# Kernel tuning notes

Measured on AMD Instinct MI355X. Metric: run time of the kernel, lower is better.

The kernel has to match this reference:

```python
import jax, jax.numpy as jnp
import numpy as np

B, C, H, W = 4, 256, 64, 64
GROUPS = 32
EPS = 1e-6
N_BITS_QKV = 8
N_BITS_SM = 8


def setup_inputs() -> dict:
    key = jax.random.key(0)
    ks = jax.random.split(key, 6)
    s = 1.0 / np.sqrt(C)
    return {
        "x": jax.random.normal(ks[0], (B, C, H, W), jnp.float32),
        "gn_scale": jnp.ones((C,), jnp.float32),
        "gn_bias": jnp.zeros((C,), jnp.float32),
        "wq": jax.random.normal(ks[1], (C, C), jnp.float32) * s,
        "bq": jnp.zeros((C,), jnp.float32),
        "wk": jax.random.normal(ks[2], (C, C), jnp.float32) * s,
        "bk": jnp.zeros((C,), jnp.float32),
        "wv": jax.random.normal(ks[3], (C, C), jnp.float32) * s,
        "bv": jnp.zeros((C,), jnp.float32),
        "wproj": jax.random.normal(ks[4], (C, C), jnp.float32) * s,
        "bproj": jnp.zeros((C,), jnp.float32),
        # per-tensor uniform-affine quantizer params (delta, zero_point)
        "dq": jnp.float32(8.0 / 255.0), "zq": jnp.float32(128.0),
        "dk": jnp.float32(8.0 / 255.0), "zk": jnp.float32(128.0),
        "dv": jnp.float32(8.0 / 255.0), "zv": jnp.float32(128.0),
        "dw": jnp.float32(1.0 / 255.0), "zw": jnp.float32(0.0),
    }


def ste_round(x):
    # round with straight-through gradient (as in round_ste of BRECQ/QDrop)
    return x + jax.lax.stop_gradient(jnp.round(x) - x)


def fake_quant(x, delta, zero_point, n_bits):
    # UniformAffineQuantizer: quant -> clamp -> dequant
    n_levels = 2 ** n_bits
    x_int = ste_round(x / delta) + zero_point
    x_q = jnp.clip(x_int, 0, n_levels - 1)
    return (x_q - zero_point) * delta


def group_norm(x, scale, bias):
    b, c, h, w = x.shape
    xg = x.reshape(b, GROUPS, (c // GROUPS) * h * w)
    mu = xg.mean(-1, keepdims=True)
    var = xg.var(-1, keepdims=True)
    xn = ((xg - mu) * jax.lax.rsqrt(var + EPS)).reshape(b, c, h, w)
    return xn * scale[None, :, None, None] + bias[None, :, None, None]


def conv1x1(x, w, b):
    # 1x1 conv == channel-mixing matmul
    return jnp.einsum('bchw,oc->bohw', x, w) + b[None, :, None, None]


def reference(x, gn_scale, gn_bias, wq, bq, wk, bk, wv, bv, wproj, bproj,
              dq, zq, dk, zk, dv, zv, dw, zw):
    h_ = group_norm(x, gn_scale, gn_bias)
    q = conv1x1(h_, wq, bq)
    k = conv1x1(h_, wk, bk)
    v = conv1x1(h_, wv, bv)
    b, c, h, w = q.shape
    hw = h * w
    q = q.reshape(b, c, hw).transpose(0, 2, 1)   # [b, hw, c]
    k = k.reshape(b, c, hw)                      # [b, c, hw]
    q = fake_quant(q, dq, zq, N_BITS_QKV)
    k = fake_quant(k, dk, zk, N_BITS_QKV)
    attn = jnp.einsum('bnc,bcm->bnm', q, k) * (c ** -0.5)  # [b, hw, hw]
    attn = jax.nn.softmax(attn, axis=2)
    v = fake_quant(v.reshape(b, c, hw), dv, zv, N_BITS_QKV)
    attn = fake_quant(attn.transpose(0, 2, 1), dw, zw, N_BITS_SM)  # [b, m, n]
    h_out = jnp.einsum('bcm,bmn->bcn', v, attn).reshape(b, c, h, w)
    return x + conv1x1(h_out, wproj, bproj)
```

## Files before the change

kernel.cpp:

```cpp
#include <hip/hip_runtime.h>


#define Bb 4
#define Cc 256
#define Nn 4096
#define NGRP 32
#define LOG2E 1.4426950408889634f

typedef unsigned short u16;
typedef unsigned int   u32;
typedef unsigned char  u8;
typedef __attribute__((ext_vector_type(8))) short bf16x8;
typedef __attribute__((ext_vector_type(4))) float f32x4;
typedef __attribute__((ext_vector_type(4))) int   i32x4;

#define MFMA16(a,b,c)    __builtin_amdgcn_mfma_f32_16x16x32_bf16((a),(b),(c),0,0,0)
#define MFMA_I8(a,b,c)   __builtin_amdgcn_mfma_i32_16x16x64_i8((a),(b),(c),0,0,0)

static __device__ __forceinline__ u16 f2bf(float x){
  u32 u = __float_as_uint(x);
  u += 0x7fffu + ((u >> 16) & 1u);
  return (u16)(u >> 16);
}
static __device__ __forceinline__ float bf2f(u16 h){ return __uint_as_float(((u32)h) << 16); }

union U64c { u16 u[4]; uint2 v; };

__global__ __launch_bounds__(256) void k_gn_stats(const float* __restrict__ x,
                                                  float* __restrict__ mu, float* __restrict__ rs){
  int bg = blockIdx.x;
  const float4* p = (const float4*)(x + (size_t)bg * (8 * Nn));
  float s = 0.f, q = 0.f;
  for (int i = threadIdx.x; i < 8*Nn/4; i += 256){
    float4 v = p[i];
    s += v.x + v.y + v.z + v.w;
    q += v.x*v.x + v.y*v.y + v.z*v.z + v.w*v.w;
  }
  __shared__ float rsum[256], rsq[256];
  rsum[threadIdx.x] = s; rsq[threadIdx.x] = q;
  __syncthreads();
  for (int off = 128; off > 0; off >>= 1){
    if (threadIdx.x < off){ rsum[threadIdx.x] += rsum[threadIdx.x+off]; rsq[threadIdx.x] += rsq[threadIdx.x+off]; }
    __syncthreads();
  }
  if (threadIdx.x == 0){
    const float inv = 1.0f / (8*Nn);
    float m = rsum[0]*inv;
    float var = rsq[0]*inv - m*m;
    mu[bg] = m; rs[bg] = rsqrtf(var + 1e-6f);
  }
}

__global__ __launch_bounds__(256) void k_wsplit(const float* __restrict__ wq, const float* __restrict__ wk,
                                                const float* __restrict__ wv, const float* __restrict__ wp,
                                                u16* __restrict__ WH, u16* __restrict__ WL){
  int gid = blockIdx.x*256 + threadIdx.x;
  int mat = gid >> 16, idx = gid & 65535;
  const float* src = (mat == 0) ? wq : (mat == 1) ? wk : (mat == 2) ? wv : wp;
  float w = src[idx];
  u16 h = f2bf(w);
  WH[gid] = h;
  WL[gid] = f2bf(w - bf2f(h));
}

__global__ __launch_bounds__(256) void k_gn_apply(const float* __restrict__ x,
                                                  const float* __restrict__ gsc, const float* __restrict__ gbi,
                                                  const float* __restrict__ mu, const float* __restrict__ rs,
                                                  u16* __restrict__ hhi, u16* __restrict__ hlo){
  int nt = blockIdx.x, ct = blockIdx.y, b = blockIdx.z;
  int n0 = nt*64, c0 = ct*64;
  __shared__ float yt[64*65];
  __shared__ float sa[64], sb[64];
  int t = threadIdx.x;
  if (t < 64){
    int c = c0 + t;
    int bg = b*NGRP + (c >> 3);
    float a = rs[bg] * gsc[c];
    sa[t] = a;
    sb[t] = gbi[c] - mu[bg]*a;
  }
  __syncthreads();
  #pragma unroll
  for (int j = 0; j < 4; ++j){
    int id = t + j*256;
    int r = id >> 4, cq = id & 15;
    float4 v = *(const float4*)(x + ((size_t)b*Cc + c0 + r)*Nn + n0 + cq*4);
    float a = sa[r], bb = sb[r];
    yt[r*65 + cq*4 + 0] = v.x*a + bb;
    yt[r*65 + cq*4 + 1] = v.y*a + bb;
    yt[r*65 + cq*4 + 2] = v.z*a + bb;
    yt[r*65 + cq*4 + 3] = v.w*a + bb;
  }
  __syncthreads();
  int nl = t >> 2, cg = (t & 3) * 16;
  size_t base = ((size_t)b*Nn + n0 + nl)*Cc + c0 + cg;
  #pragma unroll
  for (int half = 0; half < 2; ++half){
    union { u16 u[8]; uint4 v; } Ph, Pl;
    #pragma unroll
    for (int u = 0; u < 8; ++u){
      float y = yt[(cg + half*8 + u)*65 + nl];
      u16 h = f2bf(y);
      Ph.u[u] = h; Pl.u[u] = f2bf(y - bf2f(h));
    }
    *(uint4*)(hhi + base + half*8) = Ph.v;
    *(uint4*)(hlo + base + half*8) = Pl.v;
  }
}

__global__ __launch_bounds__(256) void k_convqkv(const u16* __restrict__ WH, const u16* __restrict__ WL,
                                                 const u16* __restrict__ Hhi, const u16* __restrict__ Hlo,
                                                 const float* __restrict__ bq, const float* __restrict__ bk,
                                                 const float* __restrict__ bv,
                                                 const float* __restrict__ dq, const float* __restrict__ zq,
                                                 const float* __restrict__ dk, const float* __restrict__ zk,
                                                 const float* __restrict__ dv, const float* __restrict__ zv,
                                                 u8* __restrict__ qT8, u8* __restrict__ kT8,
                                                 u8* __restrict__ v8){
  int nt = blockIdx.x, ot = blockIdx.y, b = blockIdx.z;
  __shared__ u16 Lh[64*256], Ll[64*256];
  int t = threadIdx.x, lane = t & 63, wave = t >> 6;
  int lo16 = lane & 15, quad = lane >> 4;
  int o0 = ot*64 + wave*16;

  {
    const u16* hb = Hhi + ((size_t)b*Nn + nt*64) * 256;
    const u16* lb = Hlo + ((size_t)b*Nn + nt*64) * 256;
    #pragma unroll
    for (int j = 0; j < 8; ++j){
      int id = t + j*256;
      int r = id >> 5, ch = id & 31;
      int sw = (ch ^ (r & 15)) * 8;
      *(uint4*)(Lh + r*256 + sw) = *(const uint4*)(hb + (size_t)r*256 + ch*8);
      *(uint4*)(Ll + r*256 + sw) = *(const uint4*)(lb + (size_t)r*256 + ch*8);
    }
  }
  __syncthreads();

  const float* Bs[3] = {bq, bk, bv};
  const float* Dsr[3] = {dq, dk, dv};
  const float* Zs[3] = {zq, zk, zv};

  #pragma unroll
  for (int ws = 0; ws < 3; ++ws){
    bf16x8 awh[8], awl[8];
    {
      const u16* wbh = WH + (size_t)ws*65536 + (size_t)(o0 + lo16) * 256 + quad*8;
      const u16* wbl = WL + (size_t)ws*65536 + (size_t)(o0 + lo16) * 256 + quad*8;
      #pragma unroll
      for (int k = 0; k < 8; ++k){
        awh[k] = *(const bf16x8*)(wbh + k*32);
        awl[k] = *(const bf16x8*)(wbl + k*32);
      }
    }
    f32x4 zf = {0.f,0.f,0.f,0.f};
    f32x4 acc[4] = {zf, zf, zf, zf};
    #pragma unroll
    for (int k = 0; k < 8; ++k){
      #pragma unroll
      for (int ns = 0; ns < 4; ++ns){
        int r = ns*16 + lo16;
        int ph = ((k*4 + quad) ^ (r & 15)) * 8;
        bf16x8 bh = *(const bf16x8*)(Lh + r*256 + ph);
        bf16x8 bl = *(const bf16x8*)(Ll + r*256 + ph);
        acc[ns] = MFMA16(awh[k], bh, acc[ns]);
        acc[ns] = MFMA16(awl[k], bh, acc[ns]);
        acc[ns] = MFMA16(awh[k], bl, acc[ns]);
      }
    }
    float bia[4];
    #pragma unroll
    for (int r = 0; r < 4; ++r) bia[r] = Bs[ws][o0 + quad*4 + r];
    float z = Zs[ws][0]; float invd = 1.0f / Dsr[ws][0];

    if (ws < 2){
      u8* outT = (ws == 0) ? qT8 : kT8;
      #pragma unroll
      for (int ns = 0; ns < 4; ++ns){
        int n = nt*64 + ns*16 + lo16;
        u32 w = 0;
        #pragma unroll
        for (int r = 0; r < 4; ++r){
          float v = acc[ns][r] + bia[r];
          float xq = fminf(fmaxf(rintf(v*invd) + z, 0.f), 255.f);
          int qi = (int)rintf(xq - z);
          w |= ((u32)(qi & 255)) << (8*r);
        }
        *(u32*)(outT + ((size_t)b*Nn + n)*Cc + o0 + quad*4) = w;
      }
    } else {
      #pragma unroll
      for (int ns = 0; ns < 4; ++ns){
        int n = nt*64 + ns*16 + lo16;
        #pragma unroll
        for (int r = 0; r < 4; ++r){
          float v = acc[ns][r] + bia[r];
          float xq = fminf(fmaxf(rintf(v*invd) + z, 0.f), 255.f);
          int qi = (int)rintf(xq - z);
          v8[((size_t)b*Cc + o0 + quad*4 + r)*Nn + n] = (u8)(qi & 255);
        }
      }
    }
  }
}

__global__ __launch_bounds__(256) void k_conv(const u16* __restrict__ WH, const u16* __restrict__ WL,
                                              const u16* __restrict__ Hh,
                                              const float* __restrict__ bias,
                                              const float* __restrict__ xres, float* __restrict__ outF){
  int nt = blockIdx.x, ot = blockIdx.y, b = blockIdx.z;
  __shared__ u16 Lh[64*128];
  int t = threadIdx.x, lane = t & 63, wave = t >> 6;
  int lo16 = lane & 15, quad = lane >> 4;
  int o0 = ot*64 + wave*16;

  bf16x8 awh[8], awl[8];
  {
    const u16* wbh = WH + (size_t)3*65536 + (size_t)(o0 + lo16) * 256 + quad*8;
    const u16* wbl = WL + (size_t)3*65536 + (size_t)(o0 + lo16) * 256 + quad*8;
    #pragma unroll
    for (int k = 0; k < 8; ++k){
      awh[k] = *(const bf16x8*)(wbh + k*32);
      awl[k] = *(const bf16x8*)(wbl + k*32);
    }
  }
  f32x4 zf = {0.f,0.f,0.f,0.f};
  f32x4 acc[4] = {zf, zf, zf, zf};

  const u16* hb = Hh + ((size_t)b*Nn + nt*64) * 256;
  for (int kc = 0; kc < 2; ++kc){
    __syncthreads();
    for (int id = t; id < 64*16; id += 256){
      int r = id >> 4, ch = id & 15;
      int sw = (ch ^ (r & 7)) * 8;
      *(uint4*)(Lh + r*128 + sw) = *(const uint4*)(hb + (size_t)r*256 + kc*128 + ch*8);
    }
    __syncthreads();
    #pragma unroll
    for (int k4 = 0; k4 < 4; ++k4){
      int k = kc*4 + k4;
      #pragma unroll
      for (int ns = 0; ns < 4; ++ns){
        int r = ns*16 + lo16;
        int ch = ((k4*4 + quad) ^ (r & 7)) * 8;
        bf16x8 bh = *(const bf16x8*)(Lh + r*128 + ch);
        acc[ns] = MFMA16(awh[k], bh, acc[ns]);
        acc[ns] = MFMA16(awl[k], bh, acc[ns]);
      }
    }
  }

  float bia[4];
  #pragma unroll
  for (int r = 0; r < 4; ++r) bia[r] = bias[o0 + quad*4 + r];
  #pragma unroll
  for (int ns = 0; ns < 4; ++ns){
    int n = nt*64 + ns*16 + lo16;
    #pragma unroll
    for (int r = 0; r < 4; ++r){
      size_t a = ((size_t)b*Cc + o0 + quad*4 + r)*Nn + n;
      outF[a] = xres[a] + acc[ns][r] + bia[r];
    }
  }
}

static __device__ __forceinline__ int sq4(u32 w){
  int s = 0;
  #pragma unroll
  for (int j = 0; j < 4; ++j){ int v = (int)((signed char)((w >> (8*j)) & 0xffu)); s += v*v; }
  return s;
}
static __device__ __forceinline__ int ssum4(u32 w){
  return ((int)(w << 24) >> 24) + ((int)(w << 16) >> 24) + ((int)(w << 8) >> 24) + ((int)w >> 24);
}
__global__ __launch_bounds__(256) void k_normvs(const u8* __restrict__ qT8, const u8* __restrict__ kT8,
                                                const u8* __restrict__ v8,
                                                u32* __restrict__ stat, int* __restrict__ vsum){
  if (blockIdx.x < 128){
    int gid = blockIdx.x*256 + threadIdx.x;
    int which = gid >> 14;
    int rid = gid & 16383;
    const u8* row = (which ? kT8 : qT8) + (size_t)rid * 256;
    u32 acc = 0;
    const uint4* p = (const uint4*)row;
    #pragma unroll
    for (int i = 0; i < 16; ++i){
      uint4 w = p[i];
      acc += (u32)(sq4(w.x) + sq4(w.y) + sq4(w.z) + sq4(w.w));
    }
    #pragma unroll
    for (int msk = 32; msk > 0; msk >>= 1){
      u32 o = (u32)__shfl_xor((int)acc, msk, 64);
      acc = acc > o ? acc : o;
    }
    if ((threadIdx.x & 63) == 0)
      atomicMax(&stat[which*4 + (rid >> 12)], acc);
  } else {
    int row = blockIdx.x - 128;
    uint4 w = *(const uint4*)(v8 + (size_t)row*Nn + threadIdx.x*16);
    int s = ssum4(w.x) + ssum4(w.y) + ssum4(w.z) + ssum4(w.w);
    #pragma unroll
    for (int msk = 1; msk < 64; msk <<= 1) s += __shfl_xor(s, msk, 64);
    __shared__ int r4[4];
    if ((threadIdx.x & 63) == 0) r4[threadIdx.x >> 6] = s;
    __syncthreads();
    if (threadIdx.x == 0) vsum[row] = r4[0] + r4[1] + r4[2] + r4[3];
  }
}

__global__ __launch_bounds__(1024) void k_qpv(const u8* __restrict__ qT8, const u8* __restrict__ kT8,
                                              const u8* __restrict__ v8,
                                              const u32* __restrict__ stat,
                                              const float* __restrict__ pdq, const float* __restrict__ pdk,
                                              const float* __restrict__ pdw, const float* __restrict__ pzw,
                                              const int* __restrict__ vsum,
                                              const float* __restrict__ pdv,
                                              u16* __restrict__ h2){
  int nt = blockIdx.x, b = blockIdx.y;
  __shared__ alignas(16) u8  Kt[2][64*256];
  __shared__ alignas(16) u8  Vt[2][256*64];
  __shared__ alignas(16) u32 Pt[2][64*16];
  __shared__ float Lbuf[4][4][16];
  int t = threadIdx.x, lane = t & 63, w = t >> 6;
  int lo16 = lane & 15, q = lane >> 4;
  int ms = w & 3, nsq = w >> 2;

  float sc2 = pdq[0]*pdk[0]*0.0625f*LOG2E;
  float M2 = sc2 * sqrtf((float)stat[b] * (float)stat[4+b]);
  float zw = pzw[0];

  i32x4 qf[4];
  {
    const u8* qb = qT8 + ((size_t)b*Nn + nt*64 + nsq*16 + lo16)*256;
    #pragma unroll
    for (int kk = 0; kk < 4; ++kk)
      qf[kk] = *(const i32x4*)(qb + kk*64 + q*16);
  }

  int krow = t >> 4, kch = t & 15;
  int kdst = krow*256 + ((kch ^ (krow & 15)) << 4);
  const u8* kb = kT8 + (size_t)b*Nn*256;
  int vc = t >> 2, vch = t & 3;
  int vdst = vc*64 + ((vch ^ ((vc >> 1) & 3)) << 4);
  const u8* vrow = v8 + ((size_t)(b*Cc + vc))*Nn + vch*16;

  int mrow = ms*16 + lo16;
  int kofs[4];
  #pragma unroll
  for (int kk = 0; kk < 4; ++kk) kofs[kk] = mrow*256 + (((kk*4 + q) ^ (mrow & 15)) << 4);

  float lr = 0.f;
  {
    uint4 kr = *(const uint4*)(kb + (size_t)krow*256 + kch*16);
    *(uint4*)(Kt[0] + kdst) = kr;
    kr = *(const uint4*)(kb + (size_t)(64 + krow)*256 + kch*16);
    __syncthreads();
    int cur = 0;
    for (int mt = 0; mt < 64; ++mt){
      i32x4 s = {0,0,0,0};
      #pragma unroll
      for (int kk = 0; kk < 4; ++kk)
        s = MFMA_I8(*(const i32x4*)(Kt[cur] + kofs[kk]), qf[kk], s);
      if (mt < 63){
        *(uint4*)(Kt[cur^1] + kdst) = kr;
        if (mt < 62)
          kr = *(const uint4*)(kb + (size_t)((mt+2)*64 + krow)*256 + kch*16);
      }
      #pragma unroll
      for (int r = 0; r < 4; ++r)
        lr += exp2f(fmaf((float)s[r], sc2, -M2));
      __syncthreads();
      cur ^= 1;
    }
  }
  lr += __shfl_xor(lr, 16, 64);
  lr += __shfl_xor(lr, 32, 64);
  if (lane < 16) Lbuf[nsq][ms][lo16] = lr;
  __syncthreads();
  float Ls = Lbuf[nsq][0][lo16] + Lbuf[nsq][1][lo16] + Lbuf[nsq][2][lo16] + Lbuf[nsq][3][lo16];
  float crn = __log2f(1.0f / (pdw[0] * Ls)) - M2;

  i32x4 zi = {0,0,0,0};
  i32x4 acc[4] = {zi,zi,zi,zi};
  int nrow = nsq*16 + lo16;
  int pdst = nrow*16 + ((ms ^ (nrow & 3) ^ ((nrow >> 2) & 3)) << 2) + q;
  int crv = w*16 + lo16;
  int vofs = crv*64 + ((q ^ ((crv >> 1) & 3)) << 4);
  int pofs[4];
  #pragma unroll
  for (int ns = 0; ns < 4; ++ns){
    int pr = ns*16 + lo16;
    pofs[ns] = pr*16 + ((q ^ (pr & 3) ^ ((pr >> 2) & 3)) << 2);
  }
  {
    uint4 kr = *(const uint4*)(kb + (size_t)krow*256 + kch*16);
    uint4 vr = *(const uint4*)(vrow);
    *(uint4*)(Kt[0] + kdst) = kr;
    *(uint4*)(Vt[0] + vdst) = vr;
    kr = *(const uint4*)(kb + (size_t)(64 + krow)*256 + kch*16);
    vr = *(const uint4*)(vrow + 64);
    __syncthreads();
    int cur = 0;
    for (int mt = 0; mt < 64; ++mt){
      i32x4 s = {0,0,0,0};
      #pragma unroll
      for (int kk = 0; kk < 4; ++kk)
        s = MFMA_I8(*(const i32x4*)(Kt[cur] + kofs[kk]), qf[kk], s);
      i32x4 af = *(const i32x4*)(Vt[cur] + vofs);
      if (mt < 63){
        *(uint4*)(Kt[cur^1] + kdst) = kr;
        *(uint4*)(Vt[cur^1] + vdst) = vr;
        if (mt < 62){
          kr = *(const uint4*)(kb + (size_t)((mt+2)*64 + krow)*256 + kch*16);
          vr = *(const uint4*)(vrow + (mt+2)*64);
        }
      }
      u32 wp = 0;
      #pragma unroll
      for (int r = 0; r < 4; ++r){
        float at = exp2f(fmaf((float)s[r], sc2, crn));
        float y = fminf(fmaxf(rintf(at) + zw, 0.f), 255.f);
        wp = __builtin_amdgcn_cvt_pk_u8_f32(y, (u32)r, wp);
      }
      Pt[cur][pdst] = wp ^ 0x80808080u;
      __syncthreads();
      #pragma unroll
      for (int ns = 0; ns < 4; ++ns)
        acc[ns] = MFMA_I8(af, *(const i32x4*)(Pt[cur] + pofs[ns]), acc[ns]);
      cur ^= 1;
    }
  }

  float s = pdv[0] * pdw[0];
  float corr = s * (128.0f - zw);
  int c0 = w*16 + q*4;
  float cv[4];
  #pragma unroll
  for (int r = 0; r < 4; ++r) cv[r] = corr * (float)vsum[b*Cc + c0 + r];
  #pragma unroll
  for (int ns = 0; ns < 4; ++ns){
    int n = nt*64 + ns*16 + lo16;
    U64c Uh;
    #pragma unroll
    for (int r = 0; r < 4; ++r)
      Uh.u[r] = f2bf(s*(float)acc[ns][r] + cv[r]);
    *(uint2*)(h2 + ((size_t)b*Nn + n)*Cc + c0) = Uh.v;
  }
}

extern "C" void kernel_launch(void* const* d_in, const int* in_sizes, int n_in,
                              void* d_out, int out_size, void* d_ws, size_t ws_size,
                              hipStream_t stream){
  (void)in_sizes; (void)n_in; (void)out_size; (void)ws_size;
  const float* x   = (const float*)d_in[0];
  const float* gsc = (const float*)d_in[1];
  const float* gbi = (const float*)d_in[2];
  const float* wq  = (const float*)d_in[3];
  const float* bq  = (const float*)d_in[4];
  const float* wk  = (const float*)d_in[5];
  const float* bk  = (const float*)d_in[6];
  const float* wv  = (const float*)d_in[7];
  const float* bv  = (const float*)d_in[8];
  const float* wp  = (const float*)d_in[9];
  const float* bp  = (const float*)d_in[10];
  const float* dq  = (const float*)d_in[11];
  const float* zq  = (const float*)d_in[12];
  const float* dk  = (const float*)d_in[13];
  const float* zk  = (const float*)d_in[14];
  const float* dv  = (const float*)d_in[15];
  const float* zv  = (const float*)d_in[16];
  const float* dw  = (const float*)d_in[17];
  const float* zw  = (const float*)d_in[18];
  float* out = (float*)d_out;

  const size_t SZT = (size_t)Bb*Nn*Cc;
  u16* hT_hi = (u16*)d_ws;
  u16* hT_lo = hT_hi + SZT;
  u16* h2    = hT_lo + SZT;
  u8*  qT8   = (u8*)(h2 + SZT);
  u8*  kT8   = qT8 + SZT;
  u8*  v8    = kT8 + SZT;
  u16* WH    = (u16*)(v8 + SZT);
  u16* WL    = WH + 4*65536;
  float* mu  = (float*)(WL + 4*65536);
  float* rs  = mu + 128;
  u32*  stat = (u32*)(rs + 128);
  int*  vsum = (int*)(stat + 8);

  k_gn_stats<<<dim3(Bb*NGRP), 256, 0, stream>>>(x, mu, rs);
  k_wsplit<<<dim3(1024), 256, 0, stream>>>(wq, wk, wv, wp, WH, WL);
  k_gn_apply<<<dim3(Nn/64, Cc/64, Bb), 256, 0, stream>>>(x, gsc, gbi, mu, rs, hT_hi, hT_lo);

  k_convqkv<<<dim3(Nn/64, 4, Bb), 256, 0, stream>>>(WH, WL, hT_hi, hT_lo,
                                                    bq, bk, bv, dq, zq, dk, zk, dv, zv,
                                                    qT8, kT8, v8);

  hipMemsetAsync(stat, 0, 8*sizeof(u32), stream);
  k_normvs<<<dim3(128 + Bb*Cc), 256, 0, stream>>>(qT8, kT8, v8, stat, vsum);

  k_qpv<<<dim3(Nn/64, Bb), 1024, 0, stream>>>(qT8, kT8, v8, stat, dq, dk, dw, zw, vsum, dv, h2);

  k_conv<<<dim3(Nn/64, 4, Bb), 256, 0, stream>>>(WH, WL, h2, bp, x, out);
}
```

Measured before the change: 266.8 us.

## Restructure attention kernel to 512-thread blocks with software-pipelined PV MFMAs

The fused QK-softmax-PV kernel now uses 512-thread blocks over 32 query rows, doubling the grid and targeting 4 blocks per CU via launch bounds. V fragments are read directly from global memory into registers, removing the V shared-memory tile. The PV MFMAs are deferred by one iteration so they overlap with the next QK step, and the exp pass is lagged one step as well. The QK accumulation is split into two independent MFMA chains, and exp2f is replaced with the hardware exp2 builtin. The trade-off is that K tiles are now loaded twice as often across the grid and V is read uncached from global memory.

```diff
diff --git a/kernel.cpp b/kernel.cpp
--- a/kernel.cpp
+++ b/kernel.cpp
@@ -16,6 +16,7 @@
 
 #define MFMA16(a,b,c)    __builtin_amdgcn_mfma_f32_16x16x32_bf16((a),(b),(c),0,0,0)
 #define MFMA_I8(a,b,c)   __builtin_amdgcn_mfma_i32_16x16x64_i8((a),(b),(c),0,0,0)
+#define EXP2F(x)         __builtin_amdgcn_exp2f(x)
 
 static __device__ __forceinline__ u16 f2bf(float x){
   u32 u = __float_as_uint(x);
@@ -308,7 +309,7 @@
   }
 }
 
-__global__ __launch_bounds__(1024) void k_qpv(const u8* __restrict__ qT8, const u8* __restrict__ kT8,
+__global__ __launch_bounds__(512, 4) void k_qpv(const u8* __restrict__ qT8, const u8* __restrict__ kT8,
                                               const u8* __restrict__ v8,
                                               const u32* __restrict__ stat,
                                               const float* __restrict__ pdq, const float* __restrict__ pdk,
@@ -318,9 +319,8 @@
                                               u16* __restrict__ h2){
   int nt = blockIdx.x, b = blockIdx.y;
   __shared__ alignas(16) u8  Kt[2][64*256];
-  __shared__ alignas(16) u8  Vt[2][256*64];
-  __shared__ alignas(16) u32 Pt[2][64*16];
-  __shared__ float Lbuf[4][4][16];
+  __shared__ alignas(16) u32 Pt[2][32*16];
+  __shared__ float Lbuf[2][4][16];
   int t = threadIdx.x, lane = t & 63, w = t >> 6;
   int lo16 = lane & 15, q = lane >> 4;
   int ms = w & 3, nsq = w >> 2;
@@ -331,18 +331,15 @@
 
   i32x4 qf[4];
   {
-    const u8* qb = qT8 + ((size_t)b*Nn + nt*64 + nsq*16 + lo16)*256;
+    const u8* qb = qT8 + ((size_t)b*Nn + nt*32 + nsq*16 + lo16)*256;
     #pragma unroll
     for (int kk = 0; kk < 4; ++kk)
       qf[kk] = *(const i32x4*)(qb + kk*64 + q*16);
   }
 
-  int krow = t >> 4, kch = t & 15;
-  int kdst = krow*256 + ((kch ^ (krow & 15)) << 4);
+  int kso  = (t >> 4)*256 + (t & 15)*16;
+  int kdst = (t >> 4)*256 + (((t & 15) ^ ((t >> 4) & 15)) << 4);
   const u8* kb = kT8 + (size_t)b*Nn*256;
-  int vc = t >> 2, vch = t & 3;
-  int vdst = vc*64 + ((vch ^ ((vc >> 1) & 3)) << 4);
-  const u8* vrow = v8 + ((size_t)(b*Cc + vc))*Nn + vch*16;
 
   int mrow = ms*16 + lo16;
   int kofs[4];
@@ -351,27 +348,41 @@
 
   float lr = 0.f;
   {
-    uint4 kr = *(const uint4*)(kb + (size_t)krow*256 + kch*16);
-    *(uint4*)(Kt[0] + kdst) = kr;
-    kr = *(const uint4*)(kb + (size_t)(64 + krow)*256 + kch*16);
+    uint4 kr0 = *(const uint4*)(kb + kso);
+    uint4 kr1 = *(const uint4*)(kb + kso + 8192);
+    *(uint4*)(Kt[0] + kdst) = kr0;
+    *(uint4*)(Kt[0] + kdst + 8192) = kr1;
+    kr0 = *(const uint4*)(kb + 16384 + kso);
+    kr1 = *(const uint4*)(kb + 16384 + kso + 8192);
     __syncthreads();
     int cur = 0;
+    i32x4 sp0, sp1;
     for (int mt = 0; mt < 64; ++mt){
-      i32x4 s = {0,0,0,0};
-      #pragma unroll
-      for (int kk = 0; kk < 4; ++kk)
-        s = MFMA_I8(*(const i32x4*)(Kt[cur] + kofs[kk]), qf[kk], s);
+      i32x4 sA = {0,0,0,0}, sB = {0,0,0,0};
+      sA = MFMA_I8(*(const i32x4*)(Kt[cur] + kofs[0]), qf[0], sA);
+      sB = MFMA_I8(*(const i32x4*)(Kt[cur] + kofs[1]), qf[1], sB);
+      sA = MFMA_I8(*(const i32x4*)(Kt[cur] + kofs[2]), qf[2], sA);
+      sB = MFMA_I8(*(const i32x4*)(Kt[cur] + kofs[3]), qf[3], sB);
       if (mt < 63){
-        *(uint4*)(Kt[cur^1] + kdst) = kr;
-        if (mt < 62)
-          kr = *(const uint4*)(kb + (size_t)((mt+2)*64 + krow)*256 + kch*16);
-      }
-      #pragma unroll
-      for (int r = 0; r < 4; ++r)
-        lr += exp2f(fmaf((float)s[r], sc2, -M2));
+        *(uint4*)(Kt[cur^1] + kdst) = kr0;
+        *(uint4*)(Kt[cur^1] + kdst + 8192) = kr1;
+        if (mt < 62){
+          kr0 = *(const uint4*)(kb + (size_t)(mt+2)*16384 + kso);
+          kr1 = *(const uint4*)(kb + (size_t)(mt+2)*16384 + kso + 8192);
+        }
+      }
+      if (mt > 0){
+        #pragma unroll
+        for (int r = 0; r < 4; ++r)
+          lr += EXP2F(fmaf((float)(sp0[r] + sp1[r]), sc2, -M2));
+      }
+      sp0 = sA; sp1 = sB;
       __syncthreads();
       cur ^= 1;
     }
+    #pragma unroll
+    for (int r = 0; r < 4; ++r)
+      lr += EXP2F(fmaf((float)(sp0[r] + sp1[r]), sc2, -M2));
   }
   lr += __shfl_xor(lr, 16, 64);
   lr += __shfl_xor(lr, 32, 64);
@@ -381,70 +392,93 @@
   float crn = __log2f(1.0f / (pdw[0] * Ls)) - M2;
 
   i32x4 zi = {0,0,0,0};
-  i32x4 acc[4] = {zi,zi,zi,zi};
+  i32x4 acc[2][2] = {{zi,zi},{zi,zi}};
   int nrow = nsq*16 + lo16;
   int pdst = nrow*16 + ((ms ^ (nrow & 3) ^ ((nrow >> 2) & 3)) << 2) + q;
-  int crv = w*16 + lo16;
-  int vofs = crv*64 + ((q ^ ((crv >> 1) & 3)) << 4);
-  int pofs[4];
-  #pragma unroll
-  for (int ns = 0; ns < 4; ++ns){
+  int crv0 = w*16 + lo16, crv1 = crv0 + 128;
+  const u8* vp0 = v8 + ((size_t)(b*Cc + crv0))*Nn + q*16;
+  const u8* vp1 = v8 + ((size_t)(b*Cc + crv1))*Nn + q*16;
+  int pofs[2];
+  #pragma unroll
+  for (int ns = 0; ns < 2; ++ns){
     int pr = ns*16 + lo16;
     pofs[ns] = pr*16 + ((q ^ (pr & 3) ^ ((pr >> 2) & 3)) << 2);
   }
   {
-    uint4 kr = *(const uint4*)(kb + (size_t)krow*256 + kch*16);
-    uint4 vr = *(const uint4*)(vrow);
-    *(uint4*)(Kt[0] + kdst) = kr;
-    *(uint4*)(Vt[0] + vdst) = vr;
-    kr = *(const uint4*)(kb + (size_t)(64 + krow)*256 + kch*16);
-    vr = *(const uint4*)(vrow + 64);
+    uint4 kr0 = *(const uint4*)(kb + kso);
+    uint4 kr1 = *(const uint4*)(kb + kso + 8192);
+    *(uint4*)(Kt[0] + kdst) = kr0;
+    *(uint4*)(Kt[0] + kdst + 8192) = kr1;
+    kr0 = *(const uint4*)(kb + 16384 + kso);
+    kr1 = *(const uint4*)(kb + 16384 + kso + 8192);
+    i32x4 af0 = *(const i32x4*)(vp0);
+    i32x4 af1 = *(const i32x4*)(vp1);
+    i32x4 af0p, af1p;
     __syncthreads();
     int cur = 0;
     for (int mt = 0; mt < 64; ++mt){
-      i32x4 s = {0,0,0,0};
-      #pragma unroll
-      for (int kk = 0; kk < 4; ++kk)
-        s = MFMA_I8(*(const i32x4*)(Kt[cur] + kofs[kk]), qf[kk], s);
-      i32x4 af = *(const i32x4*)(Vt[cur] + vofs);
+      i32x4 sA = {0,0,0,0}, sB = {0,0,0,0};
+      sA = MFMA_I8(*(const i32x4*)(Kt[cur] + kofs[0]), qf[0], sA);
+      sB = MFMA_I8(*(const i32x4*)(Kt[cur] + kofs[1]), qf[1], sB);
+      sA = MFMA_I8(*(const i32x4*)(Kt[cur] + kofs[2]), qf[2], sA);
+      sB = MFMA_I8(*(const i32x4*)(Kt[cur] + kofs[3]), qf[3], sB);
       if (mt < 63){
-        *(uint4*)(Kt[cur^1] + kdst) = kr;
-        *(uint4*)(Vt[cur^1] + vdst) = vr;
+        *(uint4*)(Kt[cur^1] + kdst) = kr0;
+        *(uint4*)(Kt[cur^1] + kdst + 8192) = kr1;
         if (mt < 62){
-          kr = *(const uint4*)(kb + (size_t)((mt+2)*64 + krow)*256 + kch*16);
-          vr = *(const uint4*)(vrow + (mt+2)*64);
+          kr0 = *(const uint4*)(kb + (size_t)(mt+2)*16384 + kso);
+          kr1 = *(const uint4*)(kb + (size_t)(mt+2)*16384 + kso + 8192);
         }
       }
+      if (mt > 0){
+        const i32x4 p0 = *(const i32x4*)(Pt[cur^1] + pofs[0]);
+        const i32x4 p1 = *(const i32x4*)(Pt[cur^1] + pofs[1]);
+        acc[0][0] = MFMA_I8(af0p, p0, acc[0][0]);
+        acc[0][1] = MFMA_I8(af0p, p1, acc[0][1]);
+        acc[1][0] = MFMA_I8(af1p, p0, acc[1][0]);
+        acc[1][1] = MFMA_I8(af1p, p1, acc[1][1]);
+      }
       u32 wp = 0;
       #pragma unroll
       for (int r = 0; r < 4; ++r){
-        float at = exp2f(fmaf((float)s[r], sc2, crn));
+        float at = EXP2F(fmaf((float)(sA[r] + sB[r]), sc2, crn));
         float y = fminf(fmaxf(rintf(at) + zw, 0.f), 255.f);
         wp = __builtin_amdgcn_cvt_pk_u8_f32(y, (u32)r, wp);
       }
       Pt[cur][pdst] = wp ^ 0x80808080u;
+      af0p = af0; af1p = af1;
+      if (mt < 63){
+        af0 = *(const i32x4*)(vp0 + (mt+1)*64);
+        af1 = *(const i32x4*)(vp1 + (mt+1)*64);
+      }
       __syncthreads();
-      #pragma unroll
-      for (int ns = 0; ns < 4; ++ns)
-        acc[ns] = MFMA_I8(af, *(const i32x4*)(Pt[cur] + pofs[ns]), acc[ns]);
       cur ^= 1;
     }
+    const i32x4 p0 = *(const i32x4*)(Pt[cur^1] + pofs[0]);
+    const i32x4 p1 = *(const i32x4*)(Pt[cur^1] + pofs[1]);
+    acc[0][0] = MFMA_I8(af0p, p0, acc[0][0]);
+    acc[0][1] = MFMA_I8(af0p, p1, acc[0][1]);
+    acc[1][0] = MFMA_I8(af1p, p0, acc[1][0]);
+    acc[1][1] = MFMA_I8(af1p, p1, acc[1][1]);
   }
 
   float s = pdv[0] * pdw[0];
   float corr = s * (128.0f - zw);
-  int c0 = w*16 + q*4;
-  float cv[4];
-  #pragma unroll
-  for (int r = 0; r < 4; ++r) cv[r] = corr * (float)vsum[b*Cc + c0 + r];
-  #pragma unroll
-  for (int ns = 0; ns < 4; ++ns){
-    int n = nt*64 + ns*16 + lo16;
-    U64c Uh;
-    #pragma unroll
-    for (int r = 0; r < 4; ++r)
-      Uh.u[r] = f2bf(s*(float)acc[ns][r] + cv[r]);
-    *(uint2*)(h2 + ((size_t)b*Nn + n)*Cc + c0) = Uh.v;
+  #pragma unroll
+  for (int cg = 0; cg < 2; ++cg){
+    int c0 = cg*128 + w*16 + q*4;
+    float cv[4];
+    #pragma unroll
+    for (int r = 0; r < 4; ++r) cv[r] = corr * (float)vsum[b*Cc + c0 + r];
+    #pragma unroll
+    for (int ns = 0; ns < 2; ++ns){
+      int n = nt*32 + ns*16 + lo16;
+      U64c Uh;
+      #pragma unroll
+      for (int r = 0; r < 4; ++r)
+        Uh.u[r] = f2bf(s*(float)acc[cg][ns][r] + cv[r]);
+      *(uint2*)(h2 + ((size_t)b*Nn + n)*Cc + c0) = Uh.v;
+    }
   }
 }
 
@@ -498,7 +532,7 @@
   hipMemsetAsync(stat, 0, 8*sizeof(u32), stream);
   k_normvs<<<dim3(128 + Bb*Cc), 256, 0, stream>>>(qT8, kT8, v8, stat, vsum);
 
-  k_qpv<<<dim3(Nn/64, Bb), 1024, 0, stream>>>(qT8, kT8, v8, stat, dq, dk, dw, zw, vsum, dv, h2);
+  k_qpv<<<dim3(Nn/32, Bb), 512, 0, stream>>>(qT8, kT8, v8, stat, dq, dk, dw, zw, vsum, dv, h2);
 
   k_conv<<<dim3(Nn/64, 4, Bb), 256, 0, stream>>>(WH, WL, h2, bp, x, out);
 }
```

Measured after the change: 277.1 us. +3.9%, slower.

## Software-pipeline QK, softmax-quant and PV stages; load V directly to registers

Applied to the files above, without the earlier changes.

Restructures both attention loops into a software pipeline. The exp/quantize work for tile mt-1 and the PV MFMAs for tile mt-2 now overlap with the QK MFMAs for tile mt, which leaves a single barrier per iteration instead of a barrier between producing P and consuming it. V fragments are loaded from global memory straight into registers, so the LDS V buffer and its stores go away. QK accumulation is split into two independent MFMA chains to shorten dependencies, and exp2f is swapped for the hardware exp2 builtin. The cost is more register pressure and extra prologue and epilogue code, and uncoalesced direct global V loads may add latency.

```diff
diff --git a/kernel.cpp b/kernel.cpp
--- a/kernel.cpp
+++ b/kernel.cpp
@@ -16,6 +16,7 @@
 
 #define MFMA16(a,b,c)    __builtin_amdgcn_mfma_f32_16x16x32_bf16((a),(b),(c),0,0,0)
 #define MFMA_I8(a,b,c)   __builtin_amdgcn_mfma_i32_16x16x64_i8((a),(b),(c),0,0,0)
+#define EXP2F(x)         __builtin_amdgcn_exp2f(x)
 
 static __device__ __forceinline__ u16 f2bf(float x){
   u32 u = __float_as_uint(x);
@@ -318,7 +319,6 @@
                                               u16* __restrict__ h2){
   int nt = blockIdx.x, b = blockIdx.y;
   __shared__ alignas(16) u8  Kt[2][64*256];
-  __shared__ alignas(16) u8  Vt[2][256*64];
   __shared__ alignas(16) u32 Pt[2][64*16];
   __shared__ float Lbuf[4][4][16];
   int t = threadIdx.x, lane = t & 63, w = t >> 6;
@@ -340,14 +340,13 @@
   int krow = t >> 4, kch = t & 15;
   int kdst = krow*256 + ((kch ^ (krow & 15)) << 4);
   const u8* kb = kT8 + (size_t)b*Nn*256;
-  int vc = t >> 2, vch = t & 3;
-  int vdst = vc*64 + ((vch ^ ((vc >> 1) & 3)) << 4);
-  const u8* vrow = v8 + ((size_t)(b*Cc + vc))*Nn + vch*16;
 
   int mrow = ms*16 + lo16;
   int kofs[4];
   #pragma unroll
   for (int kk = 0; kk < 4; ++kk) kofs[kk] = mrow*256 + (((kk*4 + q) ^ (mrow & 15)) << 4);
+
+  const u8* vp = v8 + ((size_t)(b*Cc + w*16 + lo16))*Nn + q*16;
 
   float lr = 0.f;
   {
@@ -356,22 +355,30 @@
     kr = *(const uint4*)(kb + (size_t)(64 + krow)*256 + kch*16);
     __syncthreads();
     int cur = 0;
+    i32x4 spA, spB;
     for (int mt = 0; mt < 64; ++mt){
-      i32x4 s = {0,0,0,0};
-      #pragma unroll
-      for (int kk = 0; kk < 4; ++kk)
-        s = MFMA_I8(*(const i32x4*)(Kt[cur] + kofs[kk]), qf[kk], s);
+      i32x4 sA = {0,0,0,0}, sB = {0,0,0,0};
+      sA = MFMA_I8(*(const i32x4*)(Kt[cur] + kofs[0]), qf[0], sA);
+      sB = MFMA_I8(*(const i32x4*)(Kt[cur] + kofs[1]), qf[1], sB);
+      sA = MFMA_I8(*(const i32x4*)(Kt[cur] + kofs[2]), qf[2], sA);
+      sB = MFMA_I8(*(const i32x4*)(Kt[cur] + kofs[3]), qf[3], sB);
       if (mt < 63){
         *(uint4*)(Kt[cur^1] + kdst) = kr;
         if (mt < 62)
           kr = *(const uint4*)(kb + (size_t)((mt+2)*64 + krow)*256 + kch*16);
       }
-      #pragma unroll
-      for (int r = 0; r < 4; ++r)
-        lr += exp2f(fmaf((float)s[r], sc2, -M2));
+      if (mt > 0){
+        #pragma unroll
+        for (int r = 0; r < 4; ++r)
+          lr += EXP2F(fmaf((float)(spA[r] + spB[r]), sc2, -M2));
+      }
+      spA = sA; spB = sB;
       __syncthreads();
       cur ^= 1;
     }
+    #pragma unroll
+    for (int r = 0; r < 4; ++r)
+      lr += EXP2F(fmaf((float)(spA[r] + spB[r]), sc2, -M2));
   }
   lr += __shfl_xor(lr, 16, 64);
   lr += __shfl_xor(lr, 32, 64);
@@ -384,8 +391,6 @@
   i32x4 acc[4] = {zi,zi,zi,zi};
   int nrow = nsq*16 + lo16;
   int pdst = nrow*16 + ((ms ^ (nrow & 3) ^ ((nrow >> 2) & 3)) << 2) + q;
-  int crv = w*16 + lo16;
-  int vofs = crv*64 + ((q ^ ((crv >> 1) & 3)) << 4);
   int pofs[4];
   #pragma unroll
   for (int ns = 0; ns < 4; ++ns){
@@ -394,41 +399,65 @@
   }
   {
     uint4 kr = *(const uint4*)(kb + (size_t)krow*256 + kch*16);
-    uint4 vr = *(const uint4*)(vrow);
     *(uint4*)(Kt[0] + kdst) = kr;
-    *(uint4*)(Vt[0] + vdst) = vr;
     kr = *(const uint4*)(kb + (size_t)(64 + krow)*256 + kch*16);
-    vr = *(const uint4*)(vrow + 64);
+    i32x4 af = *(const i32x4*)(vp);
+    i32x4 af_p, af_pp;
+    i32x4 spA, spB;
     __syncthreads();
     int cur = 0;
     for (int mt = 0; mt < 64; ++mt){
-      i32x4 s = {0,0,0,0};
-      #pragma unroll
-      for (int kk = 0; kk < 4; ++kk)
-        s = MFMA_I8(*(const i32x4*)(Kt[cur] + kofs[kk]), qf[kk], s);
-      i32x4 af = *(const i32x4*)(Vt[cur] + vofs);
+      i32x4 sA = {0,0,0,0}, sB = {0,0,0,0};
+      sA = MFMA_I8(*(const i32x4*)(Kt[cur] + kofs[0]), qf[0], sA);
+      sB = MFMA_I8(*(const i32x4*)(Kt[cur] + kofs[1]), qf[1], sB);
+      sA = MFMA_I8(*(const i32x4*)(Kt[cur] + kofs[2]), qf[2], sA);
+      sB = MFMA_I8(*(const i32x4*)(Kt[cur] + kofs[3]), qf[3], sB);
       if (mt < 63){
         *(uint4*)(Kt[cur^1] + kdst) = kr;
-        *(uint4*)(Vt[cur^1] + vdst) = vr;
-        if (mt < 62){
+        if (mt < 62)
           kr = *(const uint4*)(kb + (size_t)((mt+2)*64 + krow)*256 + kch*16);
-          vr = *(const uint4*)(vrow + (mt+2)*64);
+      }
+      if (mt > 1){
+        acc[0] = MFMA_I8(af_pp, *(const i32x4*)(Pt[mt & 1] + pofs[0]), acc[0]);
+        acc[1] = MFMA_I8(af_pp, *(const i32x4*)(Pt[mt & 1] + pofs[1]), acc[1]);
+        acc[2] = MFMA_I8(af_pp, *(const i32x4*)(Pt[mt & 1] + pofs[2]), acc[2]);
+        acc[3] = MFMA_I8(af_pp, *(const i32x4*)(Pt[mt & 1] + pofs[3]), acc[3]);
+      }
+      if (mt > 0){
+        u32 wp = 0;
+        #pragma unroll
+        for (int r = 0; r < 4; ++r){
+          float at = EXP2F(fmaf((float)(spA[r] + spB[r]), sc2, crn));
+          float y = fminf(fmaxf(rintf(at) + zw, 0.f), 255.f);
+          wp = __builtin_amdgcn_cvt_pk_u8_f32(y, (u32)r, wp);
         }
-      }
+        Pt[(mt - 1) & 1][pdst] = wp ^ 0x80808080u;
+      }
+      spA = sA; spB = sB;
+      af_pp = af_p; af_p = af;
+      if (mt < 63) af = *(const i32x4*)(vp + (size_t)(mt + 1)*64);
+      __syncthreads();
+      cur ^= 1;
+    }
+    acc[0] = MFMA_I8(af_pp, *(const i32x4*)(Pt[0] + pofs[0]), acc[0]);
+    acc[1] = MFMA_I8(af_pp, *(const i32x4*)(Pt[0] + pofs[1]), acc[1]);
+    acc[2] = MFMA_I8(af_pp, *(const i32x4*)(Pt[0] + pofs[2]), acc[2]);
+    acc[3] = MFMA_I8(af_pp, *(const i32x4*)(Pt[0] + pofs[3]), acc[3]);
+    {
       u32 wp = 0;
       #pragma unroll
       for (int r = 0; r < 4; ++r){
-        float at = exp2f(fmaf((float)s[r], sc2, crn));
+        float at = EXP2F(fmaf((float)(spA[r] + spB[r]), sc2, crn));
         float y = fminf(fmaxf(rintf(at) + zw, 0.f), 255.f);
         wp = __builtin_amdgcn_cvt_pk_u8_f32(y, (u32)r, wp);
       }
-      Pt[cur][pdst] = wp ^ 0x80808080u;
-      __syncthreads();
-      #pragma unroll
-      for (int ns = 0; ns < 4; ++ns)
-        acc[ns] = MFMA_I8(af, *(const i32x4*)(Pt[cur] + pofs[ns]), acc[ns]);
-      cur ^= 1;
-    }
+      Pt[1][pdst] = wp ^ 0x80808080u;
+    }
+    __syncthreads();
+    acc[0] = MFMA_I8(af_p, *(const i32x4*)(Pt[1] + pofs[0]), acc[0]);
+    acc[1] = MFMA_I8(af_p, *(const i32x4*)(Pt[1] + pofs[1]), acc[1]);
+    acc[2] = MFMA_I8(af_p, *(const i32x4*)(Pt[1] + pofs[2]), acc[2]);
+    acc[3] = MFMA_I8(af_p, *(const i32x4*)(Pt[1] + pofs[3]), acc[3]);
   }
 
   float s = pdv[0] * pdw[0];
```

After: 255.0 us. -4.4%, faster.

## Software-pipeline QK/PV attention loops with two key tiles per step and direct V loads

Applied to the files above, without the earlier changes.

Restructures both passes of the fused int8 attention kernel to process two 64-key tiles per iteration. The QK MFMAs are split into independent accumulator chains, and the exp/quantize of the previous step's scores is deferred so it overlaps the current MFMAs. V fragments are now read straight from global memory into registers, prefetched two steps ahead, instead of being staged through shared memory. This halves the number of barriers and uses the fast hardware exp2 builtin, at the cost of more registers, a larger P buffer and more complex prologue/epilogue code.

```diff
diff --git a/kernel.cpp b/kernel.cpp
--- a/kernel.cpp
+++ b/kernel.cpp
@@ -16,6 +16,7 @@
 
 #define MFMA16(a,b,c)    __builtin_amdgcn_mfma_f32_16x16x32_bf16((a),(b),(c),0,0,0)
 #define MFMA_I8(a,b,c)   __builtin_amdgcn_mfma_i32_16x16x64_i8((a),(b),(c),0,0,0)
+#define EXP2F(x)         __builtin_amdgcn_exp2f(x)
 
 static __device__ __forceinline__ u16 f2bf(float x){
   u32 u = __float_as_uint(x);
@@ -317,9 +318,8 @@
                                               const float* __restrict__ pdv,
                                               u16* __restrict__ h2){
   int nt = blockIdx.x, b = blockIdx.y;
-  __shared__ alignas(16) u8  Kt[2][64*256];
-  __shared__ alignas(16) u8  Vt[2][256*64];
-  __shared__ alignas(16) u32 Pt[2][64*16];
+  __shared__ alignas(16) u8  Kt[2][2][64*256];
+  __shared__ alignas(16) u32 Pt[2][2][64*16];
   __shared__ float Lbuf[4][4][16];
   int t = threadIdx.x, lane = t & 63, w = t >> 6;
   int lo16 = lane & 15, q = lane >> 4;
@@ -340,37 +340,62 @@
   int krow = t >> 4, kch = t & 15;
   int kdst = krow*256 + ((kch ^ (krow & 15)) << 4);
   const u8* kb = kT8 + (size_t)b*Nn*256;
-  int vc = t >> 2, vch = t & 3;
-  int vdst = vc*64 + ((vch ^ ((vc >> 1) & 3)) << 4);
-  const u8* vrow = v8 + ((size_t)(b*Cc + vc))*Nn + vch*16;
 
   int mrow = ms*16 + lo16;
   int kofs[4];
   #pragma unroll
   for (int kk = 0; kk < 4; ++kk) kofs[kk] = mrow*256 + (((kk*4 + q) ^ (mrow & 15)) << 4);
 
+  const u8* vp = v8 + ((size_t)(b*Cc + w*16 + lo16))*Nn + q*16;
+
   float lr = 0.f;
   {
-    uint4 kr = *(const uint4*)(kb + (size_t)krow*256 + kch*16);
-    *(uint4*)(Kt[0] + kdst) = kr;
-    kr = *(const uint4*)(kb + (size_t)(64 + krow)*256 + kch*16);
-    __syncthreads();
-    int cur = 0;
-    for (int mt = 0; mt < 64; ++mt){
-      i32x4 s = {0,0,0,0};
-      #pragma unroll
-      for (int kk = 0; kk < 4; ++kk)
-        s = MFMA_I8(*(const i32x4*)(Kt[cur] + kofs[kk]), qf[kk], s);
-      if (mt < 63){
-        *(uint4*)(Kt[cur^1] + kdst) = kr;
-        if (mt < 62)
-          kr = *(const uint4*)(kb + (size_t)((mt+2)*64 + krow)*256 + kch*16);
-      }
-      #pragma unroll
-      for (int r = 0; r < 4; ++r)
-        lr += exp2f(fmaf((float)s[r], sc2, -M2));
+    const u8* kld = kb + (size_t)krow*256 + kch*16;
+    uint4 kr0 = *(const uint4*)(kld);
+    uint4 kr1 = *(const uint4*)(kld + 16384);
+    *(uint4*)(Kt[0][0] + kdst) = kr0;
+    *(uint4*)(Kt[0][1] + kdst) = kr1;
+    kld += 2*16384;
+    kr0 = *(const uint4*)(kld);
+    kr1 = *(const uint4*)(kld + 16384);
+    kld += 2*16384;
+    __syncthreads();
+    i32x4 spA0, spB0, spA1, spB1;
+    #pragma unroll 2
+    for (int i = 0; i < 32; ++i){
+      int cur = i & 1;
+      i32x4 sA0 = {0,0,0,0}, sB0 = {0,0,0,0}, sA1 = {0,0,0,0}, sB1 = {0,0,0,0};
+      sA0 = MFMA_I8(*(const i32x4*)(Kt[cur][0] + kofs[0]), qf[0], sA0);
+      sB0 = MFMA_I8(*(const i32x4*)(Kt[cur][0] + kofs[1]), qf[1], sB0);
+      sA1 = MFMA_I8(*(const i32x4*)(Kt[cur][1] + kofs[0]), qf[0], sA1);
+      sB1 = MFMA_I8(*(const i32x4*)(Kt[cur][1] + kofs[1]), qf[1], sB1);
+      sA0 = MFMA_I8(*(const i32x4*)(Kt[cur][0] + kofs[2]), qf[2], sA0);
+      sB0 = MFMA_I8(*(const i32x4*)(Kt[cur][0] + kofs[3]), qf[3], sB0);
+      sA1 = MFMA_I8(*(const i32x4*)(Kt[cur][1] + kofs[2]), qf[2], sA1);
+      sB1 = MFMA_I8(*(const i32x4*)(Kt[cur][1] + kofs[3]), qf[3], sB1);
+      if (i < 31){
+        *(uint4*)(Kt[cur ^ 1][0] + kdst) = kr0;
+        *(uint4*)(Kt[cur ^ 1][1] + kdst) = kr1;
+        if (i < 30){
+          kr0 = *(const uint4*)(kld);
+          kr1 = *(const uint4*)(kld + 16384);
+          kld += 2*16384;
+        }
+      }
+      if (i > 0){
+        #pragma unroll
+        for (int r = 0; r < 4; ++r){
+          lr += EXP2F(fmaf((float)(spA0[r] + spB0[r]), sc2, -M2));
+          lr += EXP2F(fmaf((float)(spA1[r] + spB1[r]), sc2, -M2));
+        }
+      }
+      spA0 = sA0; spB0 = sB0; spA1 = sA1; spB1 = sB1;
       __syncthreads();
-      cur ^= 1;
+    }
+    #pragma unroll
+    for (int r = 0; r < 4; ++r){
+      lr += EXP2F(fmaf((float)(spA0[r] + spB0[r]), sc2, -M2));
+      lr += EXP2F(fmaf((float)(spA1[r] + spB1[r]), sc2, -M2));
     }
   }
   lr += __shfl_xor(lr, 16, 64);
@@ -384,8 +409,6 @@
   i32x4 acc[4] = {zi,zi,zi,zi};
   int nrow = nsq*16 + lo16;
   int pdst = nrow*16 + ((ms ^ (nrow & 3) ^ ((nrow >> 2) & 3)) << 2) + q;
-  int crv = w*16 + lo16;
-  int vofs = crv*64 + ((q ^ ((crv >> 1) & 3)) << 4);
   int pofs[4];
   #pragma unroll
   for (int ns = 0; ns < 4; ++ns){
@@ -393,42 +416,106 @@
     pofs[ns] = pr*16 + ((q ^ (pr & 3) ^ ((pr >> 2) & 3)) << 2);
   }
   {
-    uint4 kr = *(const uint4*)(kb + (size_t)krow*256 + kch*16);
-    uint4 vr = *(const uint4*)(vrow);
-    *(uint4*)(Kt[0] + kdst) = kr;
-    *(uint4*)(Vt[0] + vdst) = vr;
-    kr = *(const uint4*)(kb + (size_t)(64 + krow)*256 + kch*16);
-    vr = *(const uint4*)(vrow + 64);
-    __syncthreads();
-    int cur = 0;
-    for (int mt = 0; mt < 64; ++mt){
-      i32x4 s = {0,0,0,0};
-      #pragma unroll
-      for (int kk = 0; kk < 4; ++kk)
-        s = MFMA_I8(*(const i32x4*)(Kt[cur] + kofs[kk]), qf[kk], s);
-      i32x4 af = *(const i32x4*)(Vt[cur] + vofs);
-      if (mt < 63){
-        *(uint4*)(Kt[cur^1] + kdst) = kr;
-        *(uint4*)(Vt[cur^1] + vdst) = vr;
-        if (mt < 62){
-          kr = *(const uint4*)(kb + (size_t)((mt+2)*64 + krow)*256 + kch*16);
-          vr = *(const uint4*)(vrow + (mt+2)*64);
+    const u8* kld = kb + (size_t)krow*256 + kch*16;
+    uint4 kr0 = *(const uint4*)(kld);
+    uint4 kr1 = *(const uint4*)(kld + 16384);
+    *(uint4*)(Kt[0][0] + kdst) = kr0;
+    *(uint4*)(Kt[0][1] + kdst) = kr1;
+    kld += 2*16384;
+    kr0 = *(const uint4*)(kld);
+    kr1 = *(const uint4*)(kld + 16384);
+    kld += 2*16384;
+    const u8* vld = vp + 128;
+    i32x4 af0 = *(const i32x4*)(vp);
+    i32x4 af1 = *(const i32x4*)(vp + 64);
+    i32x4 af0p, af1p, af0pp, af1pp;
+    i32x4 spA0, spB0, spA1, spB1;
+    __syncthreads();
+    #pragma unroll 2
+    for (int i = 0; i < 32; ++i){
+      int cur = i & 1;
+      i32x4 sA0 = {0,0,0,0}, sB0 = {0,0,0,0}, sA1 = {0,0,0,0}, sB1 = {0,0,0,0};
+      sA0 = MFMA_I8(*(const i32x4*)(Kt[cur][0] + kofs[0]), qf[0], sA0);
+      sB0 = MFMA_I8(*(const i32x4*)(Kt[cur][0] + kofs[1]), qf[1], sB0);
+      sA1 = MFMA_I8(*(const i32x4*)(Kt[cur][1] + kofs[0]), qf[0], sA1);
+      sB1 = MFMA_I8(*(const i32x4*)(Kt[cur][1] + kofs[1]), qf[1], sB1);
+      sA0 = MFMA_I8(*(const i32x4*)(Kt[cur][0] + kofs[2]), qf[2], sA0);
+      sB0 = MFMA_I8(*(const i32x4*)(Kt[cur][0] + kofs[3]), qf[3], sB0);
+      sA1 = MFMA_I8(*(const i32x4*)(Kt[cur][1] + kofs[2]), qf[2], sA1);
+      sB1 = MFMA_I8(*(const i32x4*)(Kt[cur][1] + kofs[3]), qf[3], sB1);
+      if (i < 31){
+        *(uint4*)(Kt[cur ^ 1][0] + kdst) = kr0;
+        *(uint4*)(Kt[cur ^ 1][1] + kdst) = kr1;
+        if (i < 30){
+          kr0 = *(const uint4*)(kld);
+          kr1 = *(const uint4*)(kld + 16384);
+          kld += 2*16384;
         }
       }
-      u32 wp = 0;
+      if (i > 1){
+        acc[0] = MFMA_I8(af0pp, *(const i32x4*)(Pt[cur][0] + pofs[0]), acc[0]);
+        acc[1] = MFMA_I8(af0pp, *(const i32x4*)(Pt[cur][0] + pofs[1]), acc[1]);
+        acc[2] = MFMA_I8(af0pp, *(const i32x4*)(Pt[cur][0] + pofs[2]), acc[2]);
+        acc[3] = MFMA_I8(af0pp, *(const i32x4*)(Pt[cur][0] + pofs[3]), acc[3]);
+        acc[0] = MFMA_I8(af1pp, *(const i32x4*)(Pt[cur][1] + pofs[0]), acc[0]);
+        acc[1] = MFMA_I8(af1pp, *(const i32x4*)(Pt[cur][1] + pofs[1]), acc[1]);
+        acc[2] = MFMA_I8(af1pp, *(const i32x4*)(Pt[cur][1] + pofs[2]), acc[2]);
+        acc[3] = MFMA_I8(af1pp, *(const i32x4*)(Pt[cur][1] + pofs[3]), acc[3]);
+      }
+      if (i > 0){
+        u32 wp0 = 0, wp1 = 0;
+        #pragma unroll
+        for (int r = 0; r < 4; ++r){
+          float at0 = EXP2F(fmaf((float)(spA0[r] + spB0[r]), sc2, crn));
+          float y0 = fminf(fmaxf(rintf(at0) + zw, 0.f), 255.f);
+          wp0 = __builtin_amdgcn_cvt_pk_u8_f32(y0, (u32)r, wp0);
+          float at1 = EXP2F(fmaf((float)(spA1[r] + spB1[r]), sc2, crn));
+          float y1 = fminf(fmaxf(rintf(at1) + zw, 0.f), 255.f);
+          wp1 = __builtin_amdgcn_cvt_pk_u8_f32(y1, (u32)r, wp1);
+        }
+        Pt[cur ^ 1][0][pdst] = wp0 ^ 0x80808080u;
+        Pt[cur ^ 1][1][pdst] = wp1 ^ 0x80808080u;
+      }
+      spA0 = sA0; spB0 = sB0; spA1 = sA1; spB1 = sB1;
+      af0pp = af0p; af0p = af0; af1pp = af1p; af1p = af1;
+      if (i < 31){
+        af0 = *(const i32x4*)(vld);
+        af1 = *(const i32x4*)(vld + 64);
+        vld += 128;
+      }
+      __syncthreads();
+    }
+    acc[0] = MFMA_I8(af0pp, *(const i32x4*)(Pt[0][0] + pofs[0]), acc[0]);
+    acc[1] = MFMA_I8(af0pp, *(const i32x4*)(Pt[0][0] + pofs[1]), acc[1]);
+    acc[2] = MFMA_I8(af0pp, *(const i32x4*)(Pt[0][0] + pofs[2]), acc[2]);
+    acc[3] = MFMA_I8(af0pp, *(const i32x4*)(Pt[0][0] + pofs[3]), acc[3]);
+    acc[0] = MFMA_I8(af1pp, *(const i32x4*)(Pt[0][1] + pofs[0]), acc[0]);
+    acc[1] = MFMA_I8(af1pp, *(const i32x4*)(Pt[0][1] + pofs[1]), acc[1]);
+    acc[2] = MFMA_I8(af1pp, *(const i32x4*)(Pt[0][1] + pofs[2]), acc[2]);
+    acc[3] = MFMA_I8(af1pp, *(const i32x4*)(Pt[0][1] + pofs[3]), acc[3]);
+    {
+      u32 wp0 = 0, wp1 = 0;
       #pragma unroll
       for (int r = 0; r < 4; ++r){
-        float at = exp2f(fmaf((float)s[r], sc2, crn));
-        float y = fminf(fmaxf(rintf(at) + zw, 0.f), 255.f);
-        wp = __builtin_amdgcn_cvt_pk_u8_f32(y, (u32)r, wp);
-      }
-      Pt[cur][pdst] = wp ^ 0x80808080u;
-      __syncthreads();
-      #pragma unroll
-      for (int ns = 0; ns < 4; ++ns)
-        acc[ns] = MFMA_I8(af, *(const i32x4*)(Pt[cur] + pofs[ns]), acc[ns]);
-      cur ^= 1;
-    }
+        float at0 = EXP2F(fmaf((float)(spA0[r] + spB0[r]), sc2, crn));
+        float y0 = fminf(fmaxf(rintf(at0) + zw, 0.f), 255.f);
+        wp0 = __builtin_amdgcn_cvt_pk_u8_f32(y0, (u32)r, wp0);
+        float at1 = EXP2F(fmaf((float)(spA1[r] + spB1[r]), sc2, crn));
+        float y1 = fminf(fmaxf(rintf(at1) + zw, 0.f), 255.f);
+        wp1 = __builtin_amdgcn_cvt_pk_u8_f32(y1, (u32)r, wp1);
+      }
+      Pt[1][0][pdst] = wp0 ^ 0x80808080u;
+      Pt[1][1][pdst] = wp1 ^ 0x80808080u;
+    }
+    __syncthreads();
+    acc[0] = MFMA_I8(af0p, *(const i32x4*)(Pt[1][0] + pofs[0]), acc[0]);
+    acc[1] = MFMA_I8(af0p, *(const i32x4*)(Pt[1][0] + pofs[1]), acc[1]);
+    acc[2] = MFMA_I8(af0p, *(const i32x4*)(Pt[1][0] + pofs[2]), acc[2]);
+    acc[3] = MFMA_I8(af0p, *(const i32x4*)(Pt[1][0] + pofs[3]), acc[3]);
+    acc[0] = MFMA_I8(af1p, *(const i32x4*)(Pt[1][1] + pofs[0]), acc[0]);
+    acc[1] = MFMA_I8(af1p, *(const i32x4*)(Pt[1][1] + pofs[1]), acc[1]);
+    acc[2] = MFMA_I8(af1p, *(const i32x4*)(Pt[1][1] + pofs[2]), acc[2]);
+    acc[3] = MFMA_I8(af1p, *(const i32x4*)(Pt[1][1] + pofs[3]), acc[3]);
   }
 
   float s = pdv[0] * pdw[0];
```

New measurement: 246.2 us. 7.7% less time.
